# Kernel tuning notes

Hardware: AMD Instinct MI355X
Metric: run time of the kernel (lower is better)

The kernel has to match this reference:

```python
import jax, jax.numpy as jnp
import numpy as np

P = 16                     # patch size
D = 192                    # embed dim (forced by SAT d_model=192)
NHEAD = 3                  # ViT-Tiny heads
SAT_H, SAT_DK, SAT_DV = 8, 32, 32
N_SLICE = 10
PER_LI = jnp.linspace(0.1, 1.0, N_SLICE)
LN_EPS = 1e-5


def layernorm(z, g, b):
    m = z.mean(-1, keepdims=True)
    v = ((z - m) ** 2).mean(-1, keepdims=True)
    return (z - m) * jax.lax.rsqrt(v + LN_EPS) * g + b


def setup_inputs() -> dict:
    key = jax.random.key(0)
    ks = jax.random.split(key, 32)
    B, IMG, DEPTH, MLP = 128, 224, 12, 4 * D
    S = (IMG // P) ** 2 + 1  # 197 tokens
    n = lambda k, sh: jax.random.normal(k, sh, jnp.float32) * 0.02
    z = lambda sh: jnp.zeros(sh, jnp.float32)
    o = lambda sh: jnp.ones(sh, jnp.float32)
    return {
        "x": jax.random.uniform(ks[0], (B, 3, IMG, IMG), jnp.float32),
        "x_g_norm": jax.random.uniform(ks[1], (B, 1, 56, 56), jnp.float32),
        "patch_w": n(ks[2], (D, 3, P, P)), "patch_b": z((D,)),
        "cls_token": n(ks[3], (1, 1, D)), "pos_embed": n(ks[4], (1, S, D)),
        "eleva_embed": n(ks[5], (1, D)),
        "sat_wq": n(ks[6], (D, SAT_H * SAT_DK)), "sat_bq": z((SAT_H * SAT_DK,)),
        "sat_wk": n(ks[7], (D, SAT_H * SAT_DK)), "sat_bk": z((SAT_H * SAT_DK,)),
        "sat_wv": n(ks[8], (D, SAT_H * SAT_DV)), "sat_bv": z((SAT_H * SAT_DV,)),
        "sat_wo": n(ks[9], (SAT_H * SAT_DV, D)), "sat_bo": z((D,)),
        "ln1_g": o((DEPTH, D)), "ln1_b": z((DEPTH, D)),
        "qkv_w": n(ks[10], (DEPTH, D, 3 * D)), "qkv_b": z((DEPTH, 3 * D)),
        "proj_w": n(ks[11], (DEPTH, D, D)), "proj_b": z((DEPTH, D)),
        "ln2_g": o((DEPTH, D)), "ln2_b": z((DEPTH, D)),
        "fc1_w": n(ks[12], (DEPTH, D, MLP)), "fc1_b": z((DEPTH, MLP)),
        "fc2_w": n(ks[13], (DEPTH, MLP, D)), "fc2_b": z((DEPTH, D)),
        "norm_g": o((D,)), "norm_b": z((D,)),
    }


def _forward(x, x_g_norm, patch_w, patch_b, cls_token, pos_embed, eleva_embed,
             sat_wq, sat_bq, sat_wk, sat_bk, sat_wv, sat_bv, sat_wo, sat_bo,
             ln1_g, ln1_b, qkv_w, qkv_b, proj_w, proj_b, ln2_g, ln2_b,
             fc1_w, fc1_b, fc2_w, fc2_b, norm_g, norm_b):
    B = x.shape[0]
    # --- patch embed: Conv2d(3, D, kernel=P, stride=P) -> [B, N, D] ---
    feat = jax.lax.conv_general_dilated(
        x, patch_w, (P, P), 'VALID', dimension_numbers=('NCHW', 'OIHW', 'NCHW'))
    feat = feat + patch_b[None, :, None, None]
    tokens = feat.reshape(B, D, -1).transpose(0, 2, 1)          # [B, 196, D]
    tok = jnp.concatenate([jnp.broadcast_to(cls_token, (B, 1, D)), tokens], axis=1)
    tok = tok + pos_embed                                        # [B, S, D]
    S = tok.shape[1]
    # --- elevation weight per sample (vectorized bisect + linear interp) ---
    means = x_g_norm.mean(axis=(1, 2, 3))                        # [B]
    idx = jnp.clip(jnp.searchsorted(PER_LI, means, side='left'), 0, N_SLICE - 1)
    per_hi = PER_LI[idx]
    per_lo = jnp.where(idx == 0, 0.0, PER_LI[jnp.maximum(idx - 1, 0)])
    idx_f = idx.astype(jnp.float32)
    idx_inter = idx_f - (per_hi - means) / (per_hi - per_lo)
    w = jnp.where(idx == N_SLICE - 1, idx_f, idx_inter) / N_SLICE  # [B]
    # --- SAT fusion: per (batch, token) a 2-element attention over (token, ele) ---
    ele = jnp.broadcast_to(eleva_embed[0] * w[:, None, None], tok.shape)  # [B,S,D]
    at_in = jnp.stack([tok, ele], axis=2)                        # [B, S, 2, D]
    q = (at_in @ sat_wq + sat_bq).reshape(B, S, 2, SAT_H, SAT_DK)
    k = (at_in @ sat_wk + sat_bk).reshape(B, S, 2, SAT_H, SAT_DK)
    v = (at_in @ sat_wv + sat_bv).reshape(B, S, 2, SAT_H, SAT_DV)
    att = jnp.einsum('bsqhd,bskhd->bshqk', q, k) * (1.0 / np.sqrt(SAT_DK))
    att = jax.nn.softmax(att, axis=-1)
    sat_o = jnp.einsum('bshqk,bskhd->bsqhd', att, v).reshape(B, S, 2, SAT_H * SAT_DV)
    sat_o = sat_o @ sat_wo + sat_bo                              # [B, S, 2, D]
    h = sat_o[..., 0, :] + sat_o[..., 1, :]                      # [B, S, D]
    # --- ViT blocks via scan over stacked layer params ---
    hd = D // NHEAD

    def block(z, p):
        l1g, l1b, qw, qb, pw, pb, l2g, l2b, f1w, f1b, f2w, f2b = p
        y = layernorm(z, l1g, l1b)
        qkv = y @ qw + qb                                        # [B, S, 3D]
        q_, k_, v_ = jnp.split(qkv, 3, axis=-1)
        q_ = q_.reshape(B, S, NHEAD, hd)
        k_ = k_.reshape(B, S, NHEAD, hd)
        v_ = v_.reshape(B, S, NHEAD, hd)
        a = jnp.einsum('bqhd,bkhd->bhqk', q_, k_) * (hd ** -0.5)
        a = jax.nn.softmax(a, axis=-1)
        o = jnp.einsum('bhqk,bkhd->bqhd', a, v_).reshape(B, S, D)
        z = z + o @ pw + pb
        y = layernorm(z, l2g, l2b)
        z = z + jax.nn.gelu(y @ f1w + f1b, approximate=False) @ f2w + f2b
        return z, None

    h, _ = jax.lax.scan(block, h, (ln1_g, ln1_b, qkv_w, qkv_b, proj_w, proj_b,
                                   ln2_g, ln2_b, fc1_w, fc1_b, fc2_w, fc2_b))
    h = layernorm(h, norm_g, norm_b)
    return h[:, 0]                                               # [B, D] cls token


def reference(x, x_g_norm, patch_w, patch_b, cls_token, pos_embed, eleva_embed,
              sat_wq, sat_bq, sat_wk, sat_bk, sat_wv, sat_bv, sat_wo, sat_bo,
              ln1_g, ln1_b, qkv_w, qkv_b, proj_w, proj_b, ln2_g, ln2_b,
              fc1_w, fc1_b, fc2_w, fc2_b, norm_g, norm_b):
    return _forward(x, x_g_norm, patch_w, patch_b, cls_token, pos_embed, eleva_embed,
                    sat_wq, sat_bq, sat_wk, sat_bk, sat_wv, sat_bv, sat_wo, sat_bo,
                    ln1_g, ln1_b, qkv_w, qkv_b, proj_w, proj_b, ln2_g, ln2_b,
                    fc1_w, fc1_b, fc2_w, fc2_b, norm_g, norm_b)
```

## Files before the change

### kernel.cpp

```cpp
#include <hip/hip_runtime.h>


#define BATCH 128
#define SEQ 197
#define BS_ROWS (BATCH * SEQ)
#define DMODEL 192
#define NPATCH 196
#define MROWS_PATCH (BATCH * NPATCH)
#define KPATCH 768
#define MLPDIM 768
#define DEPTH 12
#define SPAD 224

typedef float f32x4 __attribute__((ext_vector_type(4)));
typedef short s16x8 __attribute__((ext_vector_type(8)));

__device__ __forceinline__ float wredSum(float v) {
#pragma unroll
  for (int o = 32; o > 0; o >>= 1) v += __shfl_xor(v, o, 64);
  return v;
}

__device__ __forceinline__ unsigned short f2bf(float f) {
  union { float f; unsigned u; } v;
  v.f = f;
  unsigned r = v.u + 0x7FFFu + ((v.u >> 16) & 1u);
  return (unsigned short)(r >> 16);
}
__device__ __forceinline__ float bf2f(unsigned short u) {
  union { unsigned u; float f; } v;
  v.u = ((unsigned)u) << 16;
  return v.f;
}

__device__ __forceinline__ int swz(int col, int row) {
  int g8 = col >> 3;
  g8 = (g8 & ~7) | ((g8 & 7) ^ (row & 7));
  return (g8 << 3) | (col & 7);
}

__device__ __forceinline__ float gelu(float x) {
  const float ax = fabsf(x) * 0.70710678118654752f;
  const float t = 1.f / (1.f + 0.3275911f * ax);
  const float y =
      t * (0.254829592f +
           t * (-0.284496736f +
                t * (1.421413741f + t * (-1.453152027f + t * 1.061405429f))));
  const float erfc_ = y * __expf(-ax * ax);
  const float cdf = (x >= 0.f) ? (1.f - 0.5f * erfc_) : (0.5f * erfc_);
  return x * cdf;
}

__global__ __launch_bounds__(256) void eleva_w_kernel(const float* __restrict__ xg,
                                                      float* __restrict__ wout) {
  const int b = blockIdx.x;
  const float* p = xg + (size_t)b * 3136;
  float s = 0.f;
  for (int i = threadIdx.x; i < 3136; i += 256) s += p[i];
  __shared__ float partial[4];
  s = wredSum(s);
  if ((threadIdx.x & 63) == 0) partial[threadIdx.x >> 6] = s;
  __syncthreads();
  if (threadIdx.x == 0) {
    float m = (partial[0] + partial[1] + partial[2] + partial[3]) / 3136.f;
    int idx = 0;
#pragma unroll
    for (int i = 0; i < 10; i++) {
      float pv = 0.1f * (float)(i + 1);
      if (pv < m) idx = i + 1;
    }
    if (idx > 9) idx = 9;
    float wv;
    if (idx == 9) {
      wv = 9.f;
    } else {
      float hi = 0.1f * (float)(idx + 1);
      float lo = (idx == 0) ? 0.f : 0.1f * (float)idx;
      wv = (float)idx - (hi - m) / (hi - lo);
    }
    wout[b] = wv / 10.f;
  }
}

__global__ __launch_bounds__(256) void wtrans_kernel(const float* __restrict__ in,
                                                     unsigned short* __restrict__ out,
                                                     int R, int C) {
  const int z = blockIdx.z;
  in += (size_t)z * R * C;
  out += (size_t)z * R * C;
  const int c0 = blockIdx.x * 32, r0 = blockIdx.y * 32;
  __shared__ float t[32][33];
  const int tr = threadIdx.x >> 3, tc = (threadIdx.x & 7) * 4;
  const float4 v = *(const float4*)(in + (size_t)(r0 + tr) * C + c0 + tc);
  t[tr][tc] = v.x; t[tr][tc + 1] = v.y; t[tr][tc + 2] = v.z; t[tr][tc + 3] = v.w;
  __syncthreads();
  ushort4 o;
  o.x = f2bf(t[tc + 0][tr]);
  o.y = f2bf(t[tc + 1][tr]);
  o.z = f2bf(t[tc + 2][tr]);
  o.w = f2bf(t[tc + 3][tr]);
  const int brow = c0 + tr;
  *(ushort4*)(out + (size_t)brow * R + swz(r0 + tc, brow)) = o;
}

__global__ __launch_bounds__(256) void convert_kernel(const float* __restrict__ in,
                                                      unsigned short* __restrict__ out, int n4,
                                                      int K) {
  const int i = blockIdx.x * 256 + threadIdx.x;
  if (i >= n4) return;
  const int flat = i * 4;
  const int row = flat / K, col = flat % K;
  const float4 v = *(const float4*)(in + flat);
  ushort4 o;
  o.x = f2bf(v.x); o.y = f2bf(v.y); o.z = f2bf(v.z); o.w = f2bf(v.w);
  *(ushort4*)(out + (size_t)row * K + swz(col, row)) = o;
}

__global__ __launch_bounds__(256) void im2col_kernel(const float* __restrict__ x,
                                                     unsigned short* __restrict__ col) {
  const int i = blockIdx.x * 256 + threadIdx.x;
  if (i >= MROWS_PATCH * KPATCH / 8) return;
  const int k = (i % 96) * 8, row = i / 96;
  const int b = row / NPATCH, p = row % NPATCH;
  const int py = p / 14, px = p % 14;
  const int c = k >> 8, r = (k >> 4) & 15, cc = k & 15;
  const float* src = x + (((size_t)b * 3 + c) * 224 + (py * 16 + r)) * 224 + (px * 16 + cc);
  const float4 v0 = *(const float4*)src;
  const float4 v1 = *(const float4*)(src + 4);
  s16x8 o;
  o[0] = (short)f2bf(v0.x); o[1] = (short)f2bf(v0.y);
  o[2] = (short)f2bf(v0.z); o[3] = (short)f2bf(v0.w);
  o[4] = (short)f2bf(v1.x); o[5] = (short)f2bf(v1.y);
  o[6] = (short)f2bf(v1.z); o[7] = (short)f2bf(v1.w);
  *(s16x8*)(col + (size_t)row * KPATCH + swz(k, row)) = o;
}

__global__ __launch_bounds__(256) void cls_kernel(const float* __restrict__ cls,
                                                  const float* __restrict__ pos,
                                                  float* __restrict__ H,
                                                  unsigned short* __restrict__ Hbf) {
  const int i = blockIdx.x * 256 + threadIdx.x;
  if (i >= BATCH * DMODEL) return;
  const int b = i / DMODEL, d = i % DMODEL;
  const float v = cls[d] + pos[d];
  const int row = b * SEQ;
  H[(size_t)row * DMODEL + d] = v;
  Hbf[(size_t)row * DMODEL + swz(d, row)] = f2bf(v);
}

__global__ __launch_bounds__(256) void ele_proj_kernel(
    const float* __restrict__ ele_emb, const float* __restrict__ wq, const float* __restrict__ bq,
    const float* __restrict__ wk, const float* __restrict__ bk,
    const float* __restrict__ wv, const float* __restrict__ bv,
    const float* __restrict__ wvec, float* __restrict__ eq, float* __restrict__ ek,
    float* __restrict__ ev, float* __restrict__ satb) {
  const int b = blockIdx.x, t = threadIdx.x;
  if (b == 0) {
    satb[t] = bq[t];
    satb[256 + t] = bk[t];
    satb[512 + t] = bv[t];
  }
  __shared__ float es[DMODEL];
  if (t < DMODEL) es[t] = ele_emb[t] * wvec[b];
  __syncthreads();
  float aq = bq[t], ak = bk[t], av = bv[t];
  for (int d = 0; d < DMODEL; d++) {
    const float e = es[d];
    aq += e * wq[d * 256 + t];
    ak += e * wk[d * 256 + t];
    av += e * wv[d * 256 + t];
  }
  eq[b * 256 + t] = aq;
  ek[b * 256 + t] = ak;
  ev[b * 256 + t] = av;
}

__global__ __launch_bounds__(256) void sat_mix_kernel(
    const unsigned short* __restrict__ qkv768, const float* __restrict__ eq,
    const float* __restrict__ ek, const float* __restrict__ ev,
    unsigned short* __restrict__ o256) {
  const int gid = blockIdx.x * 256 + threadIdx.x;
  const int tok = gid >> 3, h = gid & 7;
  if (tok >= BS_ROWS) return;
  const int b = tok / SEQ;
  const unsigned short* qp = qkv768 + (size_t)tok * 768 + h * 32;
  s16x8 qv[4], kv[4];
#pragma unroll
  for (int i0 = 0; i0 < 4; i0++) {
    qv[i0] = *(const s16x8*)(qp + i0 * 8);
    kv[i0] = *(const s16x8*)(qp + 256 + i0 * 8);
  }
  float eqa[32], eka[32];
  {
    const float4* eqp = (const float4*)(eq + b * 256 + h * 32);
    const float4* ekp = (const float4*)(ek + b * 256 + h * 32);
#pragma unroll
    for (int i0 = 0; i0 < 8; i0++) {
      const float4 a = eqp[i0], c = ekp[i0];
      eqa[i0 * 4] = a.x; eqa[i0 * 4 + 1] = a.y; eqa[i0 * 4 + 2] = a.z; eqa[i0 * 4 + 3] = a.w;
      eka[i0 * 4] = c.x; eka[i0 * 4 + 1] = c.y; eka[i0 * 4 + 2] = c.z; eka[i0 * 4 + 3] = c.w;
    }
  }
  float s00 = 0.f, s01 = 0.f, s10 = 0.f, s11 = 0.f;
#pragma unroll
  for (int d = 0; d < 32; d++) {
    const float q_ = bf2f((unsigned short)qv[d >> 3][d & 7]);
    const float k_ = bf2f((unsigned short)kv[d >> 3][d & 7]);
    s00 += q_ * k_;
    s01 += q_ * eka[d];
    s10 += eqa[d] * k_;
    s11 += eqa[d] * eka[d];
  }
  const float sc = 0.17677669529663687f;
  s00 *= sc; s01 *= sc; s10 *= sc; s11 *= sc;
  const float m0 = fmaxf(s00, s01), m1 = fmaxf(s10, s11);
  const float e00 = __expf(s00 - m0), e01 = __expf(s01 - m0);
  const float e10 = __expf(s10 - m1), e11 = __expf(s11 - m1);
  const float w0 = e00 / (e00 + e01) + e10 / (e10 + e11);
  const float w1 = e01 / (e00 + e01) + e11 / (e10 + e11);
  unsigned short* op = o256 + (size_t)tok * 256;
  const float4* evp = (const float4*)(ev + b * 256 + h * 32);
#pragma unroll
  for (int i0 = 0; i0 < 4; i0++) {
    const s16x8 vv = *(const s16x8*)(qp + 512 + i0 * 8);
    const float4 e0 = evp[i0 * 2], e1 = evp[i0 * 2 + 1];
    float ev8[8] = {e0.x, e0.y, e0.z, e0.w, e1.x, e1.y, e1.z, e1.w};
    s16x8 o;
#pragma unroll
    for (int e = 0; e < 8; e++)
      o[e] = (short)f2bf(w0 * bf2f((unsigned short)vv[e]) + w1 * ev8[e]);
    *(s16x8*)(op + swz(h * 32 + i0 * 8, tok)) = o;
  }
}

template <int EPI, bool SWZO, int BN, int BM>
__global__ __launch_bounds__(256, 4)
void gemm_mfma(const unsigned short* __restrict__ A,
               const unsigned short* __restrict__ Bt,
               const float* __restrict__ bias,
               const float* __restrict__ res,
               void* __restrict__ Cout,
               unsigned short* __restrict__ aux_hbf,
               const float* __restrict__ aux_pos,
               const float* __restrict__ lng,
               const float* __restrict__ lnb,
               int M, int N, int K, int nx) {
  constexpr int NJ = 3;
  constexpr int MI = (BM == 128) ? 4 : 2;
  constexpr bool LNF = (EPI == 5 || EPI == 6);
  constexpr int LNROWS = LNF ? BM : 1;
  int mt, nt;
  if (BM == 128) {
    const int bid = blockIdx.x;
    const int e = bid & 7, i = bid >> 3;
    nt = i % nx;
    mt = e + 8 * (i / nx);
    if (mt * BM >= M) return;
  } else {
    mt = blockIdx.y;
    nt = blockIdx.x;
  }
  __shared__ unsigned short As[BM * 64];
  __shared__ unsigned short Bs[BN * 64];
  __shared__ float2 lnbuf[4][LNROWS];
  const int tid = threadIdx.x, lane = tid & 63, w = tid >> 6;
  const int n0 = nt * BN;
  const int m0 = mt * BM;
  const int c = lane & 15, g = lane >> 4;
  const int wm = (BM == 128) ? (w >> 1) * 64 : 0;
  const int wn = (BM == 128) ? (w & 1) * 96 / 2 : w * 48;
  f32x4 acc[MI][NJ] = {};

  const int ar = (lane >> 3);
  const int acol = (lane & 7) * 8;

  for (int k0 = 0; k0 < K; k0 += 64) {
#pragma unroll
    for (int it = 0; it < BM / 32; it++) {
      const int r = w * (BM / 4) + it * 8 + ar;
      const unsigned short* gp = A + (size_t)(m0 + r) * K + k0 + acol;
      __builtin_amdgcn_global_load_lds(
          (const __attribute__((address_space(1))) unsigned int*)gp,
          (__attribute__((address_space(3))) unsigned int*)(As + (w * (BM / 4) + it * 8) * 64),
          16, 0, 0);
    }
#pragma unroll
    for (int it = 0; it < BN / 32; it++) {
      const int r = w * (BN / 4) + it * 8 + ar;
      const unsigned short* gp = Bt + (size_t)(n0 + r) * K + k0 + acol;
      __builtin_amdgcn_global_load_lds(
          (const __attribute__((address_space(1))) unsigned int*)gp,
          (__attribute__((address_space(3))) unsigned int*)(Bs + (w * (BN / 4) + it * 8) * 64),
          16, 0, 0);
    }
    __syncthreads();
#pragma unroll
    for (int kk = 0; kk < 2; kk++) {
      const int sw = (((kk * 4 + g) ^ (c & 7))) << 3;
      s16x8 af[MI], bfr[NJ];
#pragma unroll
      for (int i = 0; i < MI; i++)
        af[i] = *(const s16x8*)&As[(wm + i * 16 + c) * 64 + sw];
#pragma unroll
      for (int j = 0; j < NJ; j++)
        bfr[j] = *(const s16x8*)&Bs[(wn + j * 16 + c) * 64 + sw];
#pragma unroll
      for (int i = 0; i < MI; i++)
#pragma unroll
        for (int j = 0; j < NJ; j++)
          acc[i][j] = __builtin_amdgcn_mfma_f32_16x16x32_bf16(af[i], bfr[j], acc[i][j], 0, 0, 0);
    }
    __syncthreads();
  }

  const int ncol0 = n0 + wn + c;
  float bv[NJ];
#pragma unroll
  for (int j = 0; j < NJ; j++) bv[j] = bias[ncol0 + j * 16] * (EPI == 6 ? 2.f : 1.f);

  if constexpr (LNF) {
#pragma unroll
    for (int i = 0; i < MI; i++) {
#pragma unroll
      for (int r_ = 0; r_ < 4; r_++) {
        const int lr = wm + i * 16 + g * 4 + r_;
        const int mrow = m0 + lr;
        float s1 = 0.f, s2 = 0.f;
#pragma unroll
        for (int j = 0; j < NJ; j++) {
          float v = acc[i][j][r_] + bv[j];
          if (EPI == 5) v += res[(size_t)mrow * DMODEL + ncol0 + j * 16];
          acc[i][j][r_] = v;
          ((float*)Cout)[(size_t)mrow * DMODEL + ncol0 + j * 16] = v;
          s1 += v;
          s2 += v * v;
        }
#pragma unroll
        for (int o = 1; o <= 8; o <<= 1) {
          s1 += __shfl_xor(s1, o, 64);
          s2 += __shfl_xor(s2, o, 64);
        }
        if (c == 0) lnbuf[w][lr] = make_float2(s1, s2);
      }
    }
    __syncthreads();
    float lg[NJ], lb[NJ];
#pragma unroll
    for (int j = 0; j < NJ; j++) { lg[j] = lng[ncol0 + j * 16]; lb[j] = lnb[ncol0 + j * 16]; }
#pragma unroll
    for (int i = 0; i < MI; i++) {
#pragma unroll
      for (int r_ = 0; r_ < 4; r_++) {
        const int lr = wm + i * 16 + g * 4 + r_;
        const int mrow = m0 + lr;
        const float2 a0 = lnbuf[0][lr], a1 = lnbuf[1][lr];
        const float2 a2 = lnbuf[2][lr], a3 = lnbuf[3][lr];
        const float mean = (a0.x + a1.x + a2.x + a3.x) * (1.f / 192.f);
        const float var = (a0.y + a1.y + a2.y + a3.y) * (1.f / 192.f) - mean * mean;
        const float inv = rsqrtf(var + 1e-5f);
#pragma unroll
        for (int j = 0; j < NJ; j++) {
          const int col = ncol0 + j * 16;
          const float yn = (acc[i][j][r_] - mean) * inv * lg[j] + lb[j];
          aux_hbf[(size_t)mrow * DMODEL + swz(col, mrow)] = f2bf(yn);
        }
      }
    }
  } else if (EPI == 7 && n0 >= 384) {
#pragma unroll
    for (int i = 0; i < MI; i++) {
#pragma unroll
      for (int r_ = 0; r_ < 4; r_++) {
        const int mrow = m0 + wm + i * 16 + g * 4 + r_;
        const int b = mrow / SEQ;
        const int s = mrow - b * SEQ;
#pragma unroll
        for (int j = 0; j < NJ; j++) {
          const int vcol = ncol0 + j * 16 - 384;
          const int h = vcol >> 6, d = vcol & 63;
          aux_hbf[((size_t)((b * 3 + h) * 64 + d)) * SPAD + s] = f2bf(acc[i][j][r_] + bv[j]);
        }
      }
    }
  } else {
#pragma unroll
    for (int i = 0; i < MI; i++) {
#pragma unroll
      for (int r_ = 0; r_ < 4; r_++) {
        const int mrow = m0 + wm + i * 16 + g * 4 + r_;
        if (EPI == 4) {
          const int bb = mrow / 196;
          const int p = mrow - bb * 196;
          const int drow = mrow + bb + 1;
#pragma unroll
          for (int j = 0; j < NJ; j++) {
            const int col = ncol0 + j * 16;
            const float v = acc[i][j][r_] + bv[j] + aux_pos[(size_t)(p + 1) * DMODEL + col];
            ((float*)Cout)[(size_t)drow * DMODEL + col] = v;
            aux_hbf[(size_t)drow * DMODEL + swz(col, drow)] = f2bf(v);
          }
        } else {
#pragma unroll
          for (int j = 0; j < NJ; j++) {
            float v = acc[i][j][r_] + bv[j];
            const int col = ncol0 + j * 16;
            const size_t rowoff = (size_t)mrow * N;
            if (EPI == 1) {
              ((unsigned short*)Cout)[rowoff + (SWZO ? swz(col, mrow) : col)] = f2bf(gelu(v));
            } else {
              ((unsigned short*)Cout)[rowoff + (SWZO ? swz(col, mrow) : col)] = f2bf(v);
            }
          }
        }
      }
    }
  }
}

__global__ __launch_bounds__(256) void final_ln_kernel(const float* __restrict__ H,
                                                       const float* __restrict__ g,
                                                       const float* __restrict__ bta,
                                                       float* __restrict__ out) {
  const int w = threadIdx.x >> 6, lane = threadIdx.x & 63;
  const int bi = blockIdx.x * 4 + w;
  if (bi >= BATCH) return;
  const float* x = H + (size_t)bi * SEQ * DMODEL;
  const float x0 = x[lane], x1 = x[lane + 64], x2 = x[lane + 128];
  const float m = wredSum(x0 + x1 + x2) * (1.f / 192.f);
  const float d0 = x0 - m, d1 = x1 - m, d2 = x2 - m;
  const float v = wredSum(d0 * d0 + d1 * d1 + d2 * d2) * (1.f / 192.f);
  const float inv = rsqrtf(v + 1e-5f);
  float* y = out + (size_t)bi * DMODEL;
  y[lane] = d0 * inv * g[lane] + bta[lane];
  y[lane + 64] = d1 * inv * g[lane + 64] + bta[lane + 64];
  y[lane + 128] = d2 * inv * g[lane + 128] + bta[lane + 128];
}

__global__ __launch_bounds__(64) void attn_mfma_kernel(const unsigned short* __restrict__ qkv,
                                                       const unsigned short* __restrict__ vt,
                                                       unsigned short* __restrict__ out) {
  const int bid = blockIdx.x;
  const int bh = bid / 13, qt = bid % 13;
  const int b = bh / 3, h = bh % 3;
  const int row0 = b * SEQ;
  const int q0 = qt * 16;
  const int lane = threadIdx.x;
  const int c = lane & 15, g = lane >> 4;

  __shared__ __attribute__((aligned(16))) unsigned short P[16][232];

  const int qr = row0 + min(q0 + c, SEQ - 1);
  const unsigned short* qp = qkv + (size_t)qr * 576 + h * 64 + g * 8;
  const s16x8 qlo = *(const s16x8*)qp;
  const s16x8 qhi = *(const s16x8*)(qp + 32);

  f32x4 acc[13];
#pragma unroll
  for (int t = 0; t < 13; t++) {
    const int kr = row0 + min(t * 16 + c, SEQ - 1);
    const unsigned short* kp = qkv + (size_t)kr * 576 + 192 + h * 64 + g * 8;
    const s16x8 klo = *(const s16x8*)kp;
    const s16x8 khi = *(const s16x8*)(kp + 32);
    f32x4 z = {0.f, 0.f, 0.f, 0.f};
    z = __builtin_amdgcn_mfma_f32_16x16x32_bf16(qlo, klo, z, 0, 0, 0);
    acc[t] = __builtin_amdgcn_mfma_f32_16x16x32_bf16(qhi, khi, z, 0, 0, 0);
  }

  const bool m12 = (c >= 5);
#pragma unroll
  for (int r = 0; r < 4; r++) {
    float mx = -INFINITY;
#pragma unroll
    for (int t = 0; t < 13; t++) {
      const float v = (t == 12 && m12) ? -INFINITY : acc[t][r];
      mx = fmaxf(mx, v);
    }
#pragma unroll
    for (int o = 1; o <= 8; o <<= 1) mx = fmaxf(mx, __shfl_xor(mx, o, 64));
    const float ms = mx * 0.125f;
    float sum = 0.f;
#pragma unroll
    for (int t = 0; t < 13; t++) {
      const float e = (t == 12 && m12) ? 0.f : __expf(acc[t][r] * 0.125f - ms);
      acc[t][r] = e;
      sum += e;
    }
#pragma unroll
    for (int o = 1; o <= 8; o <<= 1) sum += __shfl_xor(sum, o, 64);
    const float inv = 1.f / sum;
#pragma unroll
    for (int t = 0; t < 13; t++) P[g * 4 + r][t * 16 + c] = f2bf(acc[t][r] * inv);
  }
  {
    unsigned short z4[4] = {0, 0, 0, 0};
    *(uint2*)&P[c][208 + g * 4] = *(uint2*)z4;
  }
  __builtin_amdgcn_s_waitcnt(0);

  f32x4 oacc[4];
#pragma unroll
  for (int dt = 0; dt < 4; dt++) oacc[dt] = (f32x4){0.f, 0.f, 0.f, 0.f};
  const unsigned short* vbase = vt + (size_t)bh * 64 * SPAD;
#pragma unroll
  for (int ch = 0; ch < 7; ch++) {
    const s16x8 pa = *(const s16x8*)&P[c][ch * 32 + g * 8];
#pragma unroll
    for (int dt = 0; dt < 4; dt++) {
      const s16x8 vb = *(const s16x8*)(vbase + (size_t)(dt * 16 + c) * SPAD + ch * 32 + g * 8);
      oacc[dt] = __builtin_amdgcn_mfma_f32_16x16x32_bf16(pa, vb, oacc[dt], 0, 0, 0);
    }
  }

#pragma unroll
  for (int dt = 0; dt < 4; dt++) {
#pragma unroll
    for (int r = 0; r < 4; r++) {
      const int q = q0 + g * 4 + r;
      if (q < SEQ) {
        const int trow = row0 + q;
        out[(size_t)trow * DMODEL + swz(h * 64 + dt * 16 + c, trow)] = f2bf(oacc[dt][r]);
      }
    }
  }
}

extern "C" void kernel_launch(void* const* d_in, const int* in_sizes, int n_in,
                              void* d_out, int out_size, void* d_ws, size_t ws_size,
                              hipStream_t stream) {
  const float* x       = (const float*)d_in[0];
  const float* xg      = (const float*)d_in[1];
  const float* patch_w = (const float*)d_in[2];
  const float* patch_b = (const float*)d_in[3];
  const float* cls_tok = (const float*)d_in[4];
  const float* pos_emb = (const float*)d_in[5];
  const float* ele_emb = (const float*)d_in[6];
  const float* sat_wq  = (const float*)d_in[7];
  const float* sat_bq  = (const float*)d_in[8];
  const float* sat_wk  = (const float*)d_in[9];
  const float* sat_bk  = (const float*)d_in[10];
  const float* sat_wv  = (const float*)d_in[11];
  const float* sat_bv  = (const float*)d_in[12];
  const float* sat_wo  = (const float*)d_in[13];
  const float* sat_bo  = (const float*)d_in[14];
  const float* ln1_g   = (const float*)d_in[15];
  const float* ln1_b   = (const float*)d_in[16];
  const float* qkv_w   = (const float*)d_in[17];
  const float* qkv_b   = (const float*)d_in[18];
  const float* proj_w  = (const float*)d_in[19];
  const float* proj_b  = (const float*)d_in[20];
  const float* ln2_g   = (const float*)d_in[21];
  const float* ln2_b   = (const float*)d_in[22];
  const float* fc1_w   = (const float*)d_in[23];
  const float* fc1_b   = (const float*)d_in[24];
  const float* fc2_w   = (const float*)d_in[25];
  const float* fc2_b   = (const float*)d_in[26];
  const float* norm_g  = (const float*)d_in[27];
  const float* norm_b  = (const float*)d_in[28];
  float* out = (float*)d_out;
  float* ws = (float*)d_ws;

  float* W_ELE = ws;
  float* EQ = ws + 256;
  float* EK = EQ + 32768;
  float* EV = EK + 32768;
  float* H = ws + 98560;
  unsigned short* Hbf   = (unsigned short*)(ws + 4940032);
  unsigned short* Ybf   = (unsigned short*)(ws + 7360768);
  unsigned short* QKVbf = (unsigned short*)(ws + 9781504);
  unsigned short* MLPbf = (unsigned short*)(ws + 17043712);
  unsigned short* VTB   = (unsigned short*)(ws + 26726656);
  unsigned short* WTS   = (unsigned short*)(ws + 29479168);
  float* SATB = ws + 32305408;
  unsigned short* ATTNbf = (unsigned short*)(ws + 32306176);

  unsigned short* qkv_wt   = WTS;
  unsigned short* proj_wt  = WTS + 1327104;
  unsigned short* fc1_wt   = WTS + 1769472;
  unsigned short* fc2_wt   = WTS + 3538944;
  unsigned short* patch_bf = WTS + 5308416;
  unsigned short* satqkv_t = WTS + 5455872;
  unsigned short* sato_t   = WTS + 5603328;

  unsigned short* COLbf   = MLPbf;
  unsigned short* SATQKV  = MLPbf;
  unsigned short* O256bf  = QKVbf;

  hipMemsetAsync(VTB, 0, (size_t)BATCH * 3 * 64 * SPAD * 2, stream);

  wtrans_kernel<<<dim3(18, 6, 12), 256, 0, stream>>>(qkv_w, qkv_wt, 192, 576);
  wtrans_kernel<<<dim3(6, 6, 12), 256, 0, stream>>>(proj_w, proj_wt, 192, 192);
  wtrans_kernel<<<dim3(24, 6, 12), 256, 0, stream>>>(fc1_w, fc1_wt, 192, 768);
  wtrans_kernel<<<dim3(6, 24, 12), 256, 0, stream>>>(fc2_w, fc2_wt, 768, 192);
  wtrans_kernel<<<dim3(8, 6, 1), 256, 0, stream>>>(sat_wq, satqkv_t, 192, 256);
  wtrans_kernel<<<dim3(8, 6, 1), 256, 0, stream>>>(sat_wk, satqkv_t + 49152, 192, 256);
  wtrans_kernel<<<dim3(8, 6, 1), 256, 0, stream>>>(sat_wv, satqkv_t + 98304, 192, 256);
  wtrans_kernel<<<dim3(6, 8, 1), 256, 0, stream>>>(sat_wo, sato_t, 256, 192);
  convert_kernel<<<144, 256, 0, stream>>>(patch_w, patch_bf, 36864, KPATCH);

  eleva_w_kernel<<<BATCH, 256, 0, stream>>>(xg, W_ELE);

  im2col_kernel<<<(MROWS_PATCH * KPATCH / 8) / 256, 256, 0, stream>>>(x, COLbf);
  gemm_mfma<4, false, 96, 128><<<400, 256, 0, stream>>>(
      COLbf, patch_bf, patch_b, nullptr, H, Hbf, pos_emb, nullptr, nullptr,
      MROWS_PATCH, DMODEL, KPATCH, 2);
  cls_kernel<<<(BATCH * DMODEL) / 256, 256, 0, stream>>>(cls_tok, pos_emb, H, Hbf);

  ele_proj_kernel<<<BATCH, 256, 0, stream>>>(ele_emb, sat_wq, sat_bq, sat_wk, sat_bk,
                                             sat_wv, sat_bv, W_ELE, EQ, EK, EV, SATB);
  gemm_mfma<0, false, 96, 128><<<1600, 256, 0, stream>>>(
      Hbf, satqkv_t, SATB, nullptr, SATQKV, nullptr, nullptr, nullptr, nullptr,
      BS_ROWS, 768, DMODEL, 8);
  sat_mix_kernel<<<BS_ROWS / 32, 256, 0, stream>>>(SATQKV, EQ, EK, EV, O256bf);
  gemm_mfma<6, false, 192, 32><<<dim3(1, 788), 256, 0, stream>>>(
      O256bf, sato_t, sat_bo, nullptr, H, Ybf, nullptr, ln1_g, ln1_b,
      BS_ROWS, DMODEL, 256, 1);

  for (int l = 0; l < DEPTH; l++) {
    gemm_mfma<7, false, 96, 128><<<1200, 256, 0, stream>>>(
        Ybf, qkv_wt + (size_t)l * 110592, qkv_b + l * 576, nullptr, QKVbf, VTB, nullptr,
        nullptr, nullptr, BS_ROWS, 576, DMODEL, 6);
    attn_mfma_kernel<<<BATCH * 3 * 13, 64, 0, stream>>>(QKVbf, VTB, ATTNbf);
    gemm_mfma<5, false, 192, 32><<<dim3(1, 788), 256, 0, stream>>>(
        ATTNbf, proj_wt + (size_t)l * 36864, proj_b + l * DMODEL, H, H, Ybf, nullptr,
        ln2_g + l * DMODEL, ln2_b + l * DMODEL, BS_ROWS, DMODEL, DMODEL, 1);
    gemm_mfma<1, true, 96, 128><<<1600, 256, 0, stream>>>(
        Ybf, fc1_wt + (size_t)l * 147456, fc1_b + l * MLPDIM, nullptr, MLPbf, nullptr, nullptr,
        nullptr, nullptr, BS_ROWS, MLPDIM, DMODEL, 8);
    const float* nlg = (l < DEPTH - 1) ? (ln1_g + (l + 1) * DMODEL) : norm_g;
    const float* nlb = (l < DEPTH - 1) ? (ln1_b + (l + 1) * DMODEL) : norm_b;
    gemm_mfma<5, false, 192, 32><<<dim3(1, 788), 256, 0, stream>>>(
        MLPbf, fc2_wt + (size_t)l * 147456, fc2_b + l * DMODEL, H, H, Ybf, nullptr,
        nlg, nlb, BS_ROWS, DMODEL, MLPDIM, 1);
  }

  final_ln_kernel<<<BATCH / 4, 256, 0, stream>>>(H, norm_g, norm_b, out);
}
```

Measured before the change: 1.724 ms.

## Fuse MLP fc1+GELU+fc2+LayerNorm into one kernel and merge weight prep launches

Replaces the separate fc1 (with GELU) and fc2 (with residual and LayerNorm) GEMM launches with a single kernel. It processes 32-row tiles, streams 64-wide hidden chunks through LDS and accumulates fc2 in registers, so the 768-wide hidden activation never goes to global memory. The cost is that every block re-streams the full fc1/fc2 weights from L2. Each chunk also runs its fc1 and fc2 stages one after the other with block barriers, and occupancy is limited by large LDS use. The eight weight-transpose launches are also collapsed into one kernel that dispatches on block index.

```diff
diff --git a/kernel.cpp b/kernel.cpp
--- a/kernel.cpp
+++ b/kernel.cpp
@@ -14,6 +14,9 @@
 
 typedef float f32x4 __attribute__((ext_vector_type(4)));
 typedef short s16x8 __attribute__((ext_vector_type(8)));
+
+#define AS1 __attribute__((address_space(1)))
+#define AS3 __attribute__((address_space(3)))
 
 __device__ __forceinline__ float wredSum(float v) {
 #pragma unroll
@@ -82,13 +85,44 @@
   }
 }
 
-__global__ __launch_bounds__(256) void wtrans_kernel(const float* __restrict__ in,
-                                                     unsigned short* __restrict__ out,
-                                                     int R, int C) {
-  const int z = blockIdx.z;
-  in += (size_t)z * R * C;
-  out += (size_t)z * R * C;
-  const int c0 = blockIdx.x * 32, r0 = blockIdx.y * 32;
+__global__ __launch_bounds__(256) void wprep_kernel(
+    const float* __restrict__ qkv_w, const float* __restrict__ proj_w,
+    const float* __restrict__ fc1_w, const float* __restrict__ fc2_w,
+    const float* __restrict__ satq, const float* __restrict__ satk,
+    const float* __restrict__ satv, const float* __restrict__ sato,
+    unsigned short* __restrict__ qkv_wt, unsigned short* __restrict__ proj_wt,
+    unsigned short* __restrict__ fc1_wt, unsigned short* __restrict__ fc2_wt,
+    unsigned short* __restrict__ satqkv_t, unsigned short* __restrict__ sato_t) {
+  int bid = blockIdx.x;
+  const float* in;
+  unsigned short* out;
+  int R, C;
+  if (bid < 1296) {
+    in = qkv_w; out = qkv_wt; R = 192; C = 576;
+  } else if ((bid -= 1296) < 432) {
+    in = proj_w; out = proj_wt; R = 192; C = 192;
+  } else if ((bid -= 432) < 1728) {
+    in = fc1_w; out = fc1_wt; R = 192; C = 768;
+  } else if ((bid -= 1728) < 1728) {
+    in = fc2_w; out = fc2_wt; R = 768; C = 192;
+  } else if ((bid -= 1728) < 48) {
+    in = satq; out = satqkv_t; R = 192; C = 256;
+  } else if ((bid -= 48) < 48) {
+    in = satk; out = satqkv_t + 49152; R = 192; C = 256;
+  } else if ((bid -= 48) < 48) {
+    in = satv; out = satqkv_t + 98304; R = 192; C = 256;
+  } else {
+    bid -= 48;
+    in = sato; out = sato_t; R = 256; C = 192;
+  }
+  const int tilesX = C >> 5;
+  const int tpm = (R >> 5) * tilesX;
+  const int mat = bid / tpm;
+  const int t_ = bid - mat * tpm;
+  const int ty = t_ / tilesX, tx = t_ - ty * tilesX;
+  in += (size_t)mat * R * C;
+  out += (size_t)mat * R * C;
+  const int c0 = tx * 32, r0 = ty * 32;
   __shared__ float t[32][33];
   const int tr = threadIdx.x >> 3, tc = (threadIdx.x & 7) * 4;
   const float4 v = *(const float4*)(in + (size_t)(r0 + tr) * C + c0 + tc);
@@ -280,18 +314,16 @@
       const int r = w * (BM / 4) + it * 8 + ar;
       const unsigned short* gp = A + (size_t)(m0 + r) * K + k0 + acol;
       __builtin_amdgcn_global_load_lds(
-          (const __attribute__((address_space(1))) unsigned int*)gp,
-          (__attribute__((address_space(3))) unsigned int*)(As + (w * (BM / 4) + it * 8) * 64),
-          16, 0, 0);
+          (const AS1 unsigned int*)gp,
+          (AS3 unsigned int*)(As + (w * (BM / 4) + it * 8) * 64), 16, 0, 0);
     }
 #pragma unroll
     for (int it = 0; it < BN / 32; it++) {
       const int r = w * (BN / 4) + it * 8 + ar;
       const unsigned short* gp = Bt + (size_t)(n0 + r) * K + k0 + acol;
       __builtin_amdgcn_global_load_lds(
-          (const __attribute__((address_space(1))) unsigned int*)gp,
-          (__attribute__((address_space(3))) unsigned int*)(Bs + (w * (BN / 4) + it * 8) * 64),
-          16, 0, 0);
+          (const AS1 unsigned int*)gp,
+          (AS3 unsigned int*)(Bs + (w * (BN / 4) + it * 8) * 64), 16, 0, 0);
     }
     __syncthreads();
 #pragma unroll
@@ -405,13 +437,160 @@
             float v = acc[i][j][r_] + bv[j];
             const int col = ncol0 + j * 16;
             const size_t rowoff = (size_t)mrow * N;
-            if (EPI == 1) {
-              ((unsigned short*)Cout)[rowoff + (SWZO ? swz(col, mrow) : col)] = f2bf(gelu(v));
-            } else {
-              ((unsigned short*)Cout)[rowoff + (SWZO ? swz(col, mrow) : col)] = f2bf(v);
-            }
+            ((unsigned short*)Cout)[rowoff + (SWZO ? swz(col, mrow) : col)] = f2bf(v);
           }
         }
+      }
+    }
+  }
+}
+
+__global__ __launch_bounds__(256, 2)
+void mlp_fused_kernel(const unsigned short* __restrict__ Yin,
+                      const unsigned short* __restrict__ w1,
+                      const unsigned short* __restrict__ w2,
+                      const float* __restrict__ b1,
+                      const float* __restrict__ b2,
+                      float* __restrict__ H,
+                      unsigned short* __restrict__ Yout,
+                      const float* __restrict__ lng,
+                      const float* __restrict__ lnb) {
+  __shared__ unsigned short Abuf[32 * 192];
+  __shared__ unsigned short W1buf[64 * 192];
+  __shared__ unsigned short W2buf[192 * 64];
+  __shared__ unsigned short Pbuf[2][32 * 64];
+  __shared__ float2 lnbuf[4][32];
+  const int tid = threadIdx.x, lane = tid & 63, w = tid >> 6;
+  const int c = lane & 15, g = lane >> 4;
+  const int m0 = blockIdx.x * 32;
+
+#pragma unroll
+  for (int it = 0; it < 3; it++) {
+    const int flat = w * 192 + it * 64 + lane;
+    const int r = flat / 24, s = flat - r * 24;
+    const unsigned short* gp = Yin + (size_t)(m0 + r) * DMODEL + s * 8;
+    __builtin_amdgcn_global_load_lds((const AS1 unsigned int*)gp,
+                                     (AS3 unsigned int*)(Abuf + flat * 8), 16, 0, 0);
+  }
+  auto stageW1 = [&](int ch) {
+#pragma unroll
+    for (int it = 0; it < 6; it++) {
+      const int flat = w * 384 + it * 64 + lane;
+      const int r = flat / 24, s = flat - r * 24;
+      const unsigned short* gp = w1 + (size_t)(ch * 64 + r) * DMODEL + s * 8;
+      __builtin_amdgcn_global_load_lds((const AS1 unsigned int*)gp,
+                                       (AS3 unsigned int*)(W1buf + flat * 8), 16, 0, 0);
+    }
+  };
+  auto stageW2 = [&](int ch) {
+#pragma unroll
+    for (int it = 0; it < 6; it++) {
+      const int flat = w * 384 + it * 64 + lane;
+      const int r = flat >> 3, s = flat & 7;
+      const unsigned short* gp = w2 + (size_t)r * MLPDIM + ch * 64 + s * 8;
+      __builtin_amdgcn_global_load_lds((const AS1 unsigned int*)gp,
+                                       (AS3 unsigned int*)(W2buf + flat * 8), 16, 0, 0);
+    }
+  };
+  stageW1(0);
+  stageW2(0);
+  __syncthreads();
+
+  f32x4 acc2[2][3] = {};
+  for (int ch = 0; ch < 12; ++ch) {
+    const float bb1 = b1[ch * 64 + w * 16 + c];
+    f32x4 a1[2] = {};
+#pragma unroll
+    for (int kk = 0; kk < 6; kk++) {
+      const int slot = kk * 4 + g;
+      const int sw1 = ((slot & ~7) | ((slot & 7) ^ (c & 7))) << 3;
+      const s16x8 bf1 = *(const s16x8*)&W1buf[(w * 16 + c) * DMODEL + sw1];
+#pragma unroll
+      for (int i = 0; i < 2; i++) {
+        const s16x8 af = *(const s16x8*)&Abuf[(i * 16 + c) * DMODEL + sw1];
+        a1[i] = __builtin_amdgcn_mfma_f32_16x16x32_bf16(af, bf1, a1[i], 0, 0, 0);
+      }
+    }
+    unsigned short* P = &Pbuf[ch & 1][0];
+#pragma unroll
+    for (int i = 0; i < 2; i++) {
+#pragma unroll
+      for (int r_ = 0; r_ < 4; r_++) {
+        const int row = i * 16 + g * 4 + r_;
+        const int col = w * 16 + c;
+        const int slotp = (col >> 3) ^ (row & 7);
+        P[row * 64 + slotp * 8 + (col & 7)] = f2bf(gelu(a1[i][r_] + bb1));
+      }
+    }
+    __syncthreads();
+    if (ch < 11) stageW1(ch + 1);
+#pragma unroll
+    for (int kk = 0; kk < 2; kk++) {
+      const int slot = kk * 4 + g;
+      const int sw2 = (slot ^ (c & 7)) << 3;
+      s16x8 af2[2], bf2[3];
+#pragma unroll
+      for (int i = 0; i < 2; i++) af2[i] = *(const s16x8*)&P[(i * 16 + c) * 64 + sw2];
+#pragma unroll
+      for (int j = 0; j < 3; j++)
+        bf2[j] = *(const s16x8*)&W2buf[(w * 48 + j * 16 + c) * 64 + sw2];
+#pragma unroll
+      for (int i = 0; i < 2; i++)
+#pragma unroll
+        for (int j = 0; j < 3; j++)
+          acc2[i][j] = __builtin_amdgcn_mfma_f32_16x16x32_bf16(af2[i], bf2[j], acc2[i][j], 0, 0, 0);
+    }
+    __syncthreads();
+    if (ch < 11) stageW2(ch + 1);
+  }
+
+  const int ncol0 = w * 48 + c;
+  float bv[3];
+#pragma unroll
+  for (int j = 0; j < 3; j++) bv[j] = b2[ncol0 + j * 16];
+#pragma unroll
+  for (int i = 0; i < 2; i++) {
+#pragma unroll
+    for (int r_ = 0; r_ < 4; r_++) {
+      const int lr = i * 16 + g * 4 + r_;
+      const int mrow = m0 + lr;
+      float s1 = 0.f, s2 = 0.f;
+#pragma unroll
+      for (int j = 0; j < 3; j++) {
+        float v = acc2[i][j][r_] + bv[j] + H[(size_t)mrow * DMODEL + ncol0 + j * 16];
+        acc2[i][j][r_] = v;
+        H[(size_t)mrow * DMODEL + ncol0 + j * 16] = v;
+        s1 += v;
+        s2 += v * v;
+      }
+#pragma unroll
+      for (int o = 1; o <= 8; o <<= 1) {
+        s1 += __shfl_xor(s1, o, 64);
+        s2 += __shfl_xor(s2, o, 64);
+      }
+      if (c == 0) lnbuf[w][lr] = make_float2(s1, s2);
+    }
+  }
+  __syncthreads();
+  float lg[3], lb[3];
+#pragma unroll
+  for (int j = 0; j < 3; j++) { lg[j] = lng[ncol0 + j * 16]; lb[j] = lnb[ncol0 + j * 16]; }
+#pragma unroll
+  for (int i = 0; i < 2; i++) {
+#pragma unroll
+    for (int r_ = 0; r_ < 4; r_++) {
+      const int lr = i * 16 + g * 4 + r_;
+      const int mrow = m0 + lr;
+      const float2 a0 = lnbuf[0][lr], a1 = lnbuf[1][lr];
+      const float2 a2 = lnbuf[2][lr], a3 = lnbuf[3][lr];
+      const float mean = (a0.x + a1.x + a2.x + a3.x) * (1.f / 192.f);
+      const float var = (a0.y + a1.y + a2.y + a3.y) * (1.f / 192.f) - mean * mean;
+      const float inv = rsqrtf(var + 1e-5f);
+#pragma unroll
+      for (int j = 0; j < 3; j++) {
+        const int col = ncol0 + j * 16;
+        const float yn = (acc2[i][j][r_] - mean) * inv * lg[j] + lb[j];
+        Yout[(size_t)mrow * DMODEL + swz(col, mrow)] = f2bf(yn);
       }
     }
   }
@@ -587,14 +766,9 @@
 
   hipMemsetAsync(VTB, 0, (size_t)BATCH * 3 * 64 * SPAD * 2, stream);
 
-  wtrans_kernel<<<dim3(18, 6, 12), 256, 0, stream>>>(qkv_w, qkv_wt, 192, 576);
-  wtrans_kernel<<<dim3(6, 6, 12), 256, 0, stream>>>(proj_w, proj_wt, 192, 192);
-  wtrans_kernel<<<dim3(24, 6, 12), 256, 0, stream>>>(fc1_w, fc1_wt, 192, 768);
-  wtrans_kernel<<<dim3(6, 24, 12), 256, 0, stream>>>(fc2_w, fc2_wt, 768, 192);
-  wtrans_kernel<<<dim3(8, 6, 1), 256, 0, stream>>>(sat_wq, satqkv_t, 192, 256);
-  wtrans_kernel<<<dim3(8, 6, 1), 256, 0, stream>>>(sat_wk, satqkv_t + 49152, 192, 256);
-  wtrans_kernel<<<dim3(8, 6, 1), 256, 0, stream>>>(sat_wv, satqkv_t + 98304, 192, 256);
-  wtrans_kernel<<<dim3(6, 8, 1), 256, 0, stream>>>(sat_wo, sato_t, 256, 192);
+  wprep_kernel<<<5376, 256, 0, stream>>>(qkv_w, proj_w, fc1_w, fc2_w, sat_wq, sat_wk,
+                                         sat_wv, sat_wo, qkv_wt, proj_wt, fc1_wt, fc2_wt,
+                                         satqkv_t, sato_t);
   convert_kernel<<<144, 256, 0, stream>>>(patch_w, patch_bf, 36864, KPATCH);
 
   eleva_w_kernel<<<BATCH, 256, 0, stream>>>(xg, W_ELE);
@@ -623,14 +797,11 @@
     gemm_mfma<5, false, 192, 32><<<dim3(1, 788), 256, 0, stream>>>(
         ATTNbf, proj_wt + (size_t)l * 36864, proj_b + l * DMODEL, H, H, Ybf, nullptr,
         ln2_g + l * DMODEL, ln2_b + l * DMODEL, BS_ROWS, DMODEL, DMODEL, 1);
-    gemm_mfma<1, true, 96, 128><<<1600, 256, 0, stream>>>(
-        Ybf, fc1_wt + (size_t)l * 147456, fc1_b + l * MLPDIM, nullptr, MLPbf, nullptr, nullptr,
-        nullptr, nullptr, BS_ROWS, MLPDIM, DMODEL, 8);
     const float* nlg = (l < DEPTH - 1) ? (ln1_g + (l + 1) * DMODEL) : norm_g;
     const float* nlb = (l < DEPTH - 1) ? (ln1_b + (l + 1) * DMODEL) : norm_b;
-    gemm_mfma<5, false, 192, 32><<<dim3(1, 788), 256, 0, stream>>>(
-        MLPbf, fc2_wt + (size_t)l * 147456, fc2_b + l * DMODEL, H, H, Ybf, nullptr,
-        nlg, nlb, BS_ROWS, DMODEL, MLPDIM, 1);
+    mlp_fused_kernel<<<788, 256, 0, stream>>>(
+        Ybf, fc1_wt + (size_t)l * 147456, fc2_wt + (size_t)l * 147456,
+        fc1_b + l * MLPDIM, fc2_b + l * DMODEL, H, Ybf, nlg, nlb);
   }
 
   final_ln_kernel<<<BATCH / 4, 256, 0, stream>>>(H, norm_g, norm_b, out);
```

Result: no change. 1.736 ms (+0.7%).
